# Optimization experiments

Measured on AMD Instinct MI355X. Metric: run time of the kernel, lower is better.

Reference implementation:

```python
import math
from itertools import product
import jax, jax.numpy as jnp
import numpy as np

# ---- static config (mirrors LPD.__init__) ----
IMG_W, IMG_H = 1920, 1080
MIN_SIZES = [[10, 16, 24], [32, 48], [64, 96], [128, 192, 256]]
STEPS = [8, 16, 32, 64]
VARIANCE = (0.1, 0.2)
CONF_THR = 0.3
NMS_THR = 0.3
TOP_K = 2000
KEEP_TOP_K = 750
BATCH = 16


def make_priors() -> np.ndarray:
    """Anchor grid in normalized (cx, cy, w, h), kornia _PriorBox order:
    per level, per cell (row-major), per min_size."""
    levels = []
    for step, mss in zip(STEPS, MIN_SIZES):
        fh, fw = math.ceil(IMG_H / step), math.ceil(IMG_W / step)
        ii, jj = np.meshgrid(np.arange(fh), np.arange(fw), indexing='ij')
        cx = (jj + 0.5) * step / IMG_W  # [fh, fw]
        cy = (ii + 0.5) * step / IMG_H
        nms_ = len(mss)
        cx = np.broadcast_to(cx[..., None], (fh, fw, nms_))
        cy = np.broadcast_to(cy[..., None], (fh, fw, nms_))
        skx = np.broadcast_to(np.array(mss, np.float64) / IMG_W, (fh, fw, nms_))
        sky = np.broadcast_to(np.array(mss, np.float64) / IMG_H, (fh, fw, nms_))
        levels.append(np.stack([cx, cy, skx, sky], -1).reshape(-1, 4))
    return np.concatenate(levels, 0).astype(np.float32)  # [N, 4]

N_PRIORS = make_priors().shape[0]  # 119130 for 1920x1080


def decode(loc, priors):
    """loc [B,N,14], priors [N,4] -> scaled [B,N,14] (x1y1x2y2 + 5 landmarks)."""
    var = jnp.asarray(VARIANCE, loc.dtype)
    p_xy, p_wh = priors[:, :2], priors[:, 2:4]
    cxcy = p_xy + loc[..., 0:2] * VARIANCE[0] * p_wh
    wh = p_wh * jnp.exp(loc[..., 2:4] * var)
    x1y1 = cxcy - wh * 0.5
    x2y2 = x1y1 + wh
    # 5 landmark points
    lmk = p_xy[None, :, None, :] + loc[..., 4:14].reshape(*loc.shape[:-1], 5, 2) * VARIANCE[0] * p_wh[None, :, None, :]
    boxes = jnp.concatenate([x1y1, x2y2, lmk.reshape(*loc.shape[:-1], 10)], -1)
    scale = jnp.tile(jnp.asarray([IMG_W, IMG_H], loc.dtype), 7)
    return boxes * scale


def nms_keep(b, s):
    """Greedy NMS. b [K,4] sorted by descending score s [K]. Returns bool keep [K]."""
    area = jnp.clip(b[:, 2] - b[:, 0], 0.0) * jnp.clip(b[:, 3] - b[:, 1], 0.0)
    lt = jnp.maximum(b[:, None, :2], b[None, :, :2])
    rb = jnp.minimum(b[:, None, 2:4], b[None, :, 2:4])
    whi = jnp.clip(rb - lt, 0.0)
    inter = whi[..., 0] * whi[..., 1]
    iou_m = inter / (area[:, None] + area[None, :] - inter + 1e-9)  # [K,K]
    K = b.shape[0]
    idx = jnp.arange(K)

    def step(active, i):
        keep_i = active[i]
        active = active & ~(keep_i & (iou_m[i] > NMS_THR) & (idx > i))
        return active, keep_i

    _, keep = jax.lax.scan(step, s > 0.0, idx)
    return keep


def setup_inputs() -> dict:
    key = jax.random.key(0)
    k1, k2, k3 = jax.random.split(key, 3)
    return {
        'loc': jax.random.normal(k1, (BATCH, N_PRIORS, 14), jnp.float32),
        'conf': jax.random.normal(k2, (BATCH, N_PRIORS, 2), jnp.float32),
        'iou': jax.random.normal(k3, (BATCH, N_PRIORS, 1), jnp.float32),
    }


def reference(loc, conf, iou):
    priors = jnp.asarray(make_priors())  # [N,4] constant
    cls = jax.nn.softmax(conf, axis=-1)[..., 1]          # [B,N]
    iou_s = jnp.clip(iou[..., 0], 0.0, 1.0)
    scores = jnp.sqrt(cls * iou_s)
    scores = jnp.where(scores >= CONF_THR, scores, 0.0)  # confidence threshold
    boxes = decode(loc, priors)                          # [B,N,14]
    top_s, top_i = jax.lax.top_k(scores, TOP_K)          # sorted desc
    boxes_k = jnp.take_along_axis(boxes, top_i[..., None], axis=1)  # [B,K,14]
    keep = jax.vmap(nms_keep)(boxes_k[..., :4], top_s)   # [B,K] bool
    keep = keep & (jnp.cumsum(keep.astype(jnp.int32), axis=-1) <= KEEP_TOP_K)
    dets = jnp.concatenate([boxes_k, (top_s * keep)[..., None]], -1)  # [B,K,15]
    return dets
```

## Files before the change

kernel.cpp:

```cpp
#include <hip/hip_runtime.h>
#include <math.h>

#define BB 16
#define TOPK 2000
#define KEEPK 750
#define CAND_CAP 4096
#define EDGE_CAP 8192
#define HIST_BINS 256
#define BIN_BASE 0x3E99u

__global__ __launch_bounds__(256) void k_scores(const float* __restrict__ conf,
                                                const float* __restrict__ iou,
                                                unsigned* __restrict__ sbits,
                                                unsigned* __restrict__ hist,
                                                unsigned* __restrict__ ccount,
                                                unsigned* __restrict__ ecount,
                                                int N, int nchunk) {
  __shared__ unsigned h[HIST_BINS];
  int b = blockIdx.y;
  int tid = threadIdx.x;
  for (int i = tid; i < HIST_BINS; i += 256) h[i] = 0;
  if (blockIdx.x == 0) {
    if (tid == 0) ccount[b] = 0;
    if (tid == 1) ecount[b] = 0;
  }
  __syncthreads();
  const float2* c2 = (const float2*)conf + (size_t)b * N;
  const float* iu = iou + (size_t)b * N;
  unsigned* sb = sbits + (size_t)b * N;
  int n0 = blockIdx.x * 4096;
#pragma unroll 4
  for (int k = 0; k < 16; ++k) {
    int n = n0 + k * 256 + tid;
    if (n < N) {
      float2 c = c2[n];
      float m = fmaxf(c.x, c.y);
      float e0 = (float)exp((double)(c.x - m));
      float e1 = (float)exp((double)(c.y - m));
      float p1 = e1 / (e0 + e1);
      float ic = fminf(fmaxf(iu[n], 0.0f), 1.0f);
      float s = sqrtf(p1 * ic);
      s = (s >= 0.3f) ? s : 0.0f;
      unsigned bits = __float_as_uint(s);
      sb[n] = bits;
      if (bits != 0u) {
        int bin = (int)(bits >> 16) - (int)BIN_BASE;
        bin = bin < 0 ? 0 : (bin > 255 ? 255 : bin);
        atomicAdd(&h[bin], 1u);
      }
    }
  }
  __syncthreads();
  unsigned* hdst = hist + ((size_t)b * nchunk + blockIdx.x) * HIST_BINS;
  for (int i = tid; i < HIST_BINS; i += 256) hdst[i] = h[i];
}

__global__ __launch_bounds__(256) void k_compact(const unsigned* __restrict__ sbits,
                                                 const unsigned* __restrict__ hist,
                                                 unsigned* __restrict__ ccount,
                                                 unsigned long long* __restrict__ ckeys,
                                                 int N, int nchunk) {
  __shared__ unsigned sT;
  __shared__ unsigned long long masks[32];
  __shared__ unsigned wioff[32];
  __shared__ unsigned blockbase;
  int b = blockIdx.y;
  int tid = threadIdx.x, lane = tid & 63, wv = tid >> 6;

  if (tid < 64) {
    const unsigned* h = hist + (size_t)b * nchunk * HIST_BINS;
    unsigned v0 = 0, v1 = 0, v2 = 0, v3 = 0;
    int b0 = 255 - (4 * lane + 0), b1 = 255 - (4 * lane + 1);
    int b2 = 255 - (4 * lane + 2), b3 = 255 - (4 * lane + 3);
    for (int c = 0; c < nchunk; ++c) {
      const unsigned* hc = h + c * HIST_BINS;
      v0 += hc[b0]; v1 += hc[b1]; v2 += hc[b2]; v3 += hc[b3];
    }
    unsigned p0 = v0, p1 = p0 + v1, p2 = p1 + v2, p3 = p2 + v3;
    unsigned tot = p3, pre = tot;
    for (int off = 1; off < 64; off <<= 1) {
      unsigned q = __shfl_up(pre, off);
      if (lane >= off) pre += q;
    }
    unsigned excl = pre - tot;
    int kk = -1;
    if (excl + p0 >= TOPK) kk = 0;
    else if (excl + p1 >= TOPK) kk = 1;
    else if (excl + p2 >= TOPK) kk = 2;
    else if (excl + p3 >= TOPK) kk = 3;
    unsigned long long m = __ballot(kk >= 0);
    int bin = 0;
    if (m != 0ull) {
      int fl = __ffsll((unsigned long long)m) - 1;
      int fk = __shfl(kk, fl);
      bin = 255 - (4 * fl + fk);
    }
    if (lane == 0) sT = ((unsigned)(BIN_BASE + (unsigned)bin)) << 16;
  }
  __syncthreads();
  unsigned T = sT;

  const unsigned* sb = sbits + (size_t)b * N;
  int n0 = blockIdx.x * 2048;
  unsigned v[8];
  unsigned long long mk[8];
#pragma unroll
  for (int k = 0; k < 8; ++k) {
    int n = n0 + k * 256 + tid;
    v[k] = (n < N) ? sb[n] : 0u;
    bool p = v[k] >= T;
    mk[k] = __ballot(p);
    if (lane == 0) masks[k * 4 + wv] = mk[k];
  }
  __syncthreads();
  if (tid < 64) {
    unsigned c = (tid < 32) ? (unsigned)__popcll(masks[tid]) : 0u;
    unsigned pre = c;
    for (int off = 1; off < 64; off <<= 1) {
      unsigned q = __shfl_up(pre, off);
      if (lane >= off) pre += q;
    }
    if (tid < 32) wioff[tid] = pre - c;
    if (tid == 31) blockbase = atomicAdd(&ccount[b], pre);
  }
  __syncthreads();
  unsigned base = blockbase;
#pragma unroll
  for (int k = 0; k < 8; ++k) {
    if ((mk[k] >> lane) & 1ull) {
      unsigned pos = base + wioff[k * 4 + wv] +
                     (unsigned)__popcll(mk[k] & ((1ull << lane) - 1ull));
      if (pos < CAND_CAP) {
        int n = n0 + k * 256 + tid;
        ckeys[(size_t)b * CAND_CAP + pos] =
            ((unsigned long long)v[k] << 32) | (unsigned)(~(unsigned)n);
      }
    }
  }
}

__global__ __launch_bounds__(256) void k_sort1(const unsigned* __restrict__ ccount,
                                               unsigned long long* __restrict__ ckeys) {
  __shared__ unsigned long long s[1024];
  int b = blockIdx.x >> 2, chunk = blockIdx.x & 3;
  bool asc = (chunk & 1) != 0;
  int t = threadIdx.x;
  unsigned c = ccount[b];
  if (c > CAND_CAP) c = CAND_CAP;
  unsigned long long* base = ckeys + (size_t)b * CAND_CAP + chunk * 1024;
  int goff = chunk * 1024;
  unsigned long long key[4];
#pragma unroll
  for (int e = 0; e < 4; ++e) {
    int g = goff + 4 * t + e;
    key[e] = (g < (int)c) ? base[4 * t + e] : 0ull;
  }
  for (int k = 2; k <= 1024; k <<= 1) {
    for (int j = k >> 1; j > 0; j >>= 1) {
      if (j >= 256) {
        __syncthreads();
#pragma unroll
        for (int e = 0; e < 4; ++e) s[4 * t + e] = key[e];
        __syncthreads();
        int pbase = (4 * t) ^ j;
        bool own_lo = ((4 * t) & j) == 0;
        bool dir = (((4 * t) & k) == 0) != asc;
        bool keep_max = (own_lo == dir);
#pragma unroll
        for (int e = 0; e < 4; ++e) {
          unsigned long long o = s[pbase + e];
          unsigned long long mx = key[e] > o ? key[e] : o;
          unsigned long long mn = key[e] > o ? o : key[e];
          key[e] = keep_max ? mx : mn;
        }
      } else if (j >= 4) {
        int d = j >> 2;
        bool own_lo = (t & d) == 0;
        bool dir = (((4 * t) & k) == 0) != asc;
        bool keep_max = (own_lo == dir);
#pragma unroll
        for (int e = 0; e < 4; ++e) {
          unsigned long long o = __shfl_xor(key[e], d, 64);
          unsigned long long mx = key[e] > o ? key[e] : o;
          unsigned long long mn = key[e] > o ? o : key[e];
          key[e] = keep_max ? mx : mn;
        }
      } else {
#pragma unroll
        for (int e = 0; e < 4; ++e) {
          int p = e ^ j;
          if (p > e) {
            int i = 4 * t + e;
            bool dir = (((i & k) == 0) != asc);
            bool need = dir ? (key[e] < key[p]) : (key[e] > key[p]);
            if (need) { unsigned long long tmp = key[e]; key[e] = key[p]; key[p] = tmp; }
          }
        }
      }
    }
  }
#pragma unroll
  for (int e = 0; e < 4; ++e) base[4 * t + e] = key[e];
}

__global__ __launch_bounds__(1024) void k_sort2_decode(
    const unsigned long long* __restrict__ ckeys, const float* __restrict__ loc,
    float* __restrict__ top_s, float* __restrict__ out,
    float4* __restrict__ boxes4, int N) {
  __shared__ unsigned long long s[CAND_CAP];
  int b = blockIdx.x;
  int t = threadIdx.x;
  const unsigned long long* src = ckeys + (size_t)b * CAND_CAP;
  unsigned long long key[4];
#pragma unroll
  for (int e = 0; e < 4; ++e) key[e] = src[4 * t + e];
  for (int k = 2048; k <= CAND_CAP; k <<= 1) {
    for (int j = k >> 1; j > 0; j >>= 1) {
      if (j >= 256) {
        __syncthreads();
#pragma unroll
        for (int e = 0; e < 4; ++e) s[4 * t + e] = key[e];
        __syncthreads();
        int pbase = (4 * t) ^ j;
        bool own_lo = ((4 * t) & j) == 0;
        bool dir = ((4 * t) & k) == 0;
        bool keep_max = (own_lo == dir);
#pragma unroll
        for (int e = 0; e < 4; ++e) {
          unsigned long long o = s[pbase + e];
          unsigned long long mx = key[e] > o ? key[e] : o;
          unsigned long long mn = key[e] > o ? o : key[e];
          key[e] = keep_max ? mx : mn;
        }
      } else if (j >= 4) {
        int d = j >> 2;
        bool own_lo = (t & d) == 0;
        bool dir = ((4 * t) & k) == 0;
        bool keep_max = (own_lo == dir);
#pragma unroll
        for (int e = 0; e < 4; ++e) {
          unsigned long long o = __shfl_xor(key[e], d, 64);
          unsigned long long mx = key[e] > o ? key[e] : o;
          unsigned long long mn = key[e] > o ? o : key[e];
          key[e] = keep_max ? mx : mn;
        }
      } else {
#pragma unroll
        for (int e = 0; e < 4; ++e) {
          int p = e ^ j;
          if (p > e) {
            int i = 4 * t + e;
            bool dir = ((i & k) == 0);
            bool need = dir ? (key[e] < key[p]) : (key[e] > key[p]);
            if (need) { unsigned long long tmp = key[e]; key[e] = key[p]; key[p] = tmp; }
          }
        }
      }
    }
  }
  if (t < TOPK / 4) {
#pragma unroll
    for (int e = 0; e < 4; ++e) {
      int r = 4 * t + e;
      unsigned long long kk = key[e];
      float sv = __uint_as_float((unsigned)(kk >> 32));
      top_s[b * TOPK + r] = sv;
      unsigned idxu = ~(unsigned)kk;
      if (idxu >= (unsigned)N) idxu = 0;
      int i = (int)idxu;
      int off, fw, st, nm, lvl;
      if (i < 97200)       { lvl = 0; off = 0;      fw = 240; st = 8;  nm = 3; }
      else if (i < 113520) { lvl = 1; off = 97200;  fw = 120; st = 16; nm = 2; }
      else if (i < 117600) { lvl = 2; off = 113520; fw = 60;  st = 32; nm = 2; }
      else                 { lvl = 3; off = 117600; fw = 30;  st = 64; nm = 3; }
      int tt = i - off;
      int cell = tt / nm;
      int kms = tt - cell * nm;
      int row = cell / fw;
      int col = cell - row * fw;
      int msv = (lvl == 0) ? (kms == 0 ? 10 : (kms == 1 ? 16 : 24))
              : (lvl == 1) ? (kms == 0 ? 32 : 48)
              : (lvl == 2) ? (kms == 0 ? 64 : 96)
                           : (kms == 0 ? 128 : (kms == 1 ? 192 : 256));
      float cx  = (float)(((double)col + 0.5) * (double)st / 1920.0);
      float cy  = (float)(((double)row + 0.5) * (double)st / 1080.0);
      float skx = (float)((double)msv / 1920.0);
      float sky = (float)((double)msv / 1080.0);
      const float2* lp2 = (const float2*)(loc + ((size_t)b * N + (size_t)i) * 14);
      float l[14];
#pragma unroll
      for (int q = 0; q < 7; ++q) { float2 v = lp2[q]; l[2 * q] = v.x; l[2 * q + 1] = v.y; }
      float cx2 = cx + (l[0] * 0.1f) * skx;
      float cy2 = cy + (l[1] * 0.1f) * sky;
      float wx = skx * expf(l[2] * 0.1f);
      float wy = sky * expf(l[3] * 0.2f);
      float x1 = cx2 - wx * 0.5f, y1 = cy2 - wy * 0.5f;
      float x2 = x1 + wx, y2 = y1 + wy;
      float X1 = x1 * 1920.0f, Y1 = y1 * 1080.0f, X2 = x2 * 1920.0f, Y2 = y2 * 1080.0f;
      float* o = out + ((size_t)b * TOPK + r) * 15;
      o[0] = X1; o[1] = Y1; o[2] = X2; o[3] = Y2;
#pragma unroll
      for (int q = 0; q < 5; ++q) {
        o[4 + 2 * q] = (cx + (l[4 + 2 * q] * 0.1f) * skx) * 1920.0f;
        o[5 + 2 * q] = (cy + (l[5 + 2 * q] * 0.1f) * sky) * 1080.0f;
      }
      boxes4[b * TOPK + r] = make_float4(X1, Y1, X2, Y2);
    }
  }
}

__global__ __launch_bounds__(128) void k_edges(const float4* __restrict__ boxes4,
                                               unsigned* __restrict__ ecount,
                                               unsigned* __restrict__ edges) {
  __shared__ float bx1[128], by1[128], bx2[128], by2[128], bta[128];
  __shared__ unsigned loc_e[1024];
  __shared__ unsigned lcnt, gbase;
  int b = blockIdx.y;
  int t = blockIdx.x;
  int it = 0;
  while ((it + 1) * (it + 2) / 2 <= t) ++it;
  int jt = t - it * (it + 1) / 2;
  int tid = threadIdx.x;
  if (tid == 0) lcnt = 0;
  int j0 = jt * 128;
  {
    int j = j0 + tid;
    if (j < TOPK) {
      float4 Bj = boxes4[b * TOPK + j];
      bx1[tid] = Bj.x; by1[tid] = Bj.y; bx2[tid] = Bj.z; by2[tid] = Bj.w;
      bta[tid] = 0.3f * (fmaxf(Bj.z - Bj.x, 0.f) * fmaxf(Bj.w - Bj.y, 0.f));
    } else {
      bx1[tid] = 1e30f; by1[tid] = 1e30f; bx2[tid] = -1e30f; by2[tid] = -1e30f;
      bta[tid] = 0.f;
    }
  }
  __syncthreads();
  int i = it * 128 + tid;
  int jmax = 0;
  float4 A4 = make_float4(0, 0, 0, 0);
  float taA = 0.f;
  if (i < TOPK) {
    A4 = boxes4[b * TOPK + i];
    taA = 0.3f * (fmaxf(A4.z - A4.x, 0.f) * fmaxf(A4.w - A4.y, 0.f));
    jmax = i - j0; if (jmax > 128) jmax = 128;
  }
  for (int c = 0; c < jmax; ++c) {
    float xx1 = fmaxf(A4.x, bx1[c]), yy1 = fmaxf(A4.y, by1[c]);
    float xx2 = fminf(A4.z, bx2[c]), yy2 = fminf(A4.w, by2[c]);
    float w = fmaxf(xx2 - xx1, 0.f), h = fmaxf(yy2 - yy1, 0.f);
    float inter = w * h;
    if (inter * 1.3f > taA + bta[c] + 3e-10f) {
      unsigned p = atomicAdd(&lcnt, 1u);
      if (p < 1024u) loc_e[p] = ((unsigned)i << 16) | (unsigned)(j0 + c);
    }
  }
  __syncthreads();
  unsigned cnt = lcnt > 1024u ? 1024u : lcnt;
  if (tid == 0 && cnt) gbase = atomicAdd(&ecount[b], cnt);
  __syncthreads();
  if (cnt) {
    unsigned* dst = edges + (size_t)b * EDGE_CAP;
    for (unsigned e = tid; e < cnt; e += 128) {
      unsigned p = gbase + e;
      if (p < EDGE_CAP) dst[p] = loc_e[e];
    }
  }
}

__global__ __launch_bounds__(256) void k_nms(const float* __restrict__ top_s,
                                             const unsigned* __restrict__ ecount,
                                             const unsigned* __restrict__ edges,
                                             float* __restrict__ out) {
  int b = blockIdx.x;
  __shared__ unsigned long long A[32], K[32], S[32];
  __shared__ unsigned pref[32];
  __shared__ unsigned ecache[4096];
  __shared__ int changed;
  int tid = threadIdx.x, lane = tid & 63, wv = tid >> 6;
  for (int base = 0; base < 2048; base += 256) {
    int i = base + tid;
    bool act = (i < TOPK) && (top_s[b * TOPK + i] > 0.0f);
    unsigned long long m = __ballot(act);
    if (lane == 0) { int w = (base >> 6) + wv; A[w] = m; K[w] = m; }
  }
  unsigned E = ecount[b];
  if (E > EDGE_CAP) E = EDGE_CAP;
  unsigned Ec = E > 4096u ? 4096u : E;
  for (unsigned e = tid; e < Ec; e += 256) ecache[e] = edges[(size_t)b * EDGE_CAP + e];
  __syncthreads();
  for (int it = 0; it < 32; ++it) {
    if (tid == 0) changed = 0;
    if (tid < 32) S[tid] = 0ull;
    __syncthreads();
    for (unsigned e = tid; e < Ec; e += 256) {
      unsigned v = ecache[e];
      unsigned i = v >> 16, j = v & 0xFFFFu;
      if ((K[j >> 6] >> (j & 63)) & 1ull) atomicOr(&S[i >> 6], 1ull << (i & 63));
    }
    for (unsigned e = 4096u + tid; e < E; e += 256) {
      unsigned v = edges[(size_t)b * EDGE_CAP + e];
      unsigned i = v >> 16, j = v & 0xFFFFu;
      if ((K[j >> 6] >> (j & 63)) & 1ull) atomicOr(&S[i >> 6], 1ull << (i & 63));
    }
    __syncthreads();
    if (tid < 32) {
      unsigned long long nk = A[tid] & ~S[tid];
      if (nk != K[tid]) { K[tid] = nk; changed = 1; }
    }
    __syncthreads();
    if (!changed) break;
  }
  if (tid == 0) {
    unsigned acc = 0;
    for (int w = 0; w < 32; ++w) { pref[w] = acc; acc += (unsigned)__popcll(K[w]); }
  }
  __syncthreads();
  for (int base = 0; base < 2048; base += 256) {
    int i = base + tid;
    if (i < TOPK) {
      int w = i >> 6;
      unsigned long long bit = (K[w] >> (i & 63)) & 1ull;
      unsigned rank = pref[w] + (unsigned)__popcll(K[w] & ((1ull << (i & 63)) - 1ull)) +
                      (unsigned)bit;
      float sv = top_s[b * TOPK + i];
      out[((size_t)b * TOPK + i) * 15 + 14] = (bit && rank <= KEEPK) ? sv : 0.0f;
    }
  }
}

extern "C" void kernel_launch(void* const* d_in, const int* in_sizes, int n_in,
                              void* d_out, int out_size, void* d_ws, size_t ws_size,
                              hipStream_t stream) {
  const float* loc  = (const float*)d_in[0];
  const float* conf = (const float*)d_in[1];
  const float* iou  = (const float*)d_in[2];
  float* out = (float*)d_out;
  int N = in_sizes[2] / BB;
  int nchunk = (N + 4095) / 4096;

  char* ws = (char*)d_ws;
  size_t off = 0;
  unsigned* ccount = (unsigned*)(ws + off); off += 64;
  unsigned* ecount = (unsigned*)(ws + off); off += 64;
  off = (off + 255) & ~(size_t)255;
  unsigned* hist   = (unsigned*)(ws + off); off += (size_t)BB * nchunk * HIST_BINS * 4;
  unsigned* sbits  = (unsigned*)(ws + off); off += (size_t)BB * N * 4;
  off = (off + 15) & ~(size_t)15;
  unsigned long long* ckeys = (unsigned long long*)(ws + off); off += (size_t)BB * CAND_CAP * 8;
  float* top_s = (float*)(ws + off);       off += (size_t)BB * TOPK * 4;
  off = (off + 15) & ~(size_t)15;
  float4* boxes4 = (float4*)(ws + off);    off += (size_t)BB * TOPK * 16;
  unsigned* edges = (unsigned*)(ws + off); off += (size_t)BB * EDGE_CAP * 4;

  k_scores<<<dim3(nchunk, BB), 256, 0, stream>>>(conf, iou, sbits, hist, ccount,
                                                 ecount, N, nchunk);
  k_compact<<<dim3((N + 2047) / 2048, BB), 256, 0, stream>>>(sbits, hist, ccount,
                                                             ckeys, N, nchunk);
  k_sort1<<<BB * 4, 256, 0, stream>>>(ccount, ckeys);
  k_sort2_decode<<<BB, 1024, 0, stream>>>(ckeys, loc, top_s, out, boxes4, N);
  k_edges<<<dim3(136, BB), 128, 0, stream>>>(boxes4, ecount, edges);
  k_nms<<<BB, 256, 0, stream>>>(top_s, ecount, edges, out);
}
```

Measured before the change: 270.2 us.

## Fuse edge construction and NMS via last-block atomic counter; spread decode across threads

```diff
diff --git a/kernel.cpp b/kernel.cpp
--- a/kernel.cpp
+++ b/kernel.cpp
@@ -15,6 +15,7 @@
                                                 unsigned* __restrict__ hist,
                                                 unsigned* __restrict__ ccount,
                                                 unsigned* __restrict__ ecount,
+                                                unsigned* __restrict__ tdone,
                                                 int N, int nchunk) {
   __shared__ unsigned h[HIST_BINS];
   int b = blockIdx.y;
@@ -23,6 +24,7 @@
   if (blockIdx.x == 0) {
     if (tid == 0) ccount[b] = 0;
     if (tid == 1) ecount[b] = 0;
+    if (tid == 2) tdone[b] = 0;
   }
   __syncthreads();
   const float2* c2 = (const float2*)conf + (size_t)b * N;
@@ -258,63 +260,67 @@
       }
     }
   }
-  if (t < TOPK / 4) {
-#pragma unroll
-    for (int e = 0; e < 4; ++e) {
-      int r = 4 * t + e;
-      unsigned long long kk = key[e];
-      float sv = __uint_as_float((unsigned)(kk >> 32));
-      top_s[b * TOPK + r] = sv;
-      unsigned idxu = ~(unsigned)kk;
-      if (idxu >= (unsigned)N) idxu = 0;
-      int i = (int)idxu;
-      int off, fw, st, nm, lvl;
-      if (i < 97200)       { lvl = 0; off = 0;      fw = 240; st = 8;  nm = 3; }
-      else if (i < 113520) { lvl = 1; off = 97200;  fw = 120; st = 16; nm = 2; }
-      else if (i < 117600) { lvl = 2; off = 113520; fw = 60;  st = 32; nm = 2; }
-      else                 { lvl = 3; off = 117600; fw = 30;  st = 64; nm = 3; }
-      int tt = i - off;
-      int cell = tt / nm;
-      int kms = tt - cell * nm;
-      int row = cell / fw;
-      int col = cell - row * fw;
-      int msv = (lvl == 0) ? (kms == 0 ? 10 : (kms == 1 ? 16 : 24))
-              : (lvl == 1) ? (kms == 0 ? 32 : 48)
-              : (lvl == 2) ? (kms == 0 ? 64 : 96)
-                           : (kms == 0 ? 128 : (kms == 1 ? 192 : 256));
-      float cx  = (float)(((double)col + 0.5) * (double)st / 1920.0);
-      float cy  = (float)(((double)row + 0.5) * (double)st / 1080.0);
-      float skx = (float)((double)msv / 1920.0);
-      float sky = (float)((double)msv / 1080.0);
-      const float2* lp2 = (const float2*)(loc + ((size_t)b * N + (size_t)i) * 14);
-      float l[14];
-#pragma unroll
-      for (int q = 0; q < 7; ++q) { float2 v = lp2[q]; l[2 * q] = v.x; l[2 * q + 1] = v.y; }
-      float cx2 = cx + (l[0] * 0.1f) * skx;
-      float cy2 = cy + (l[1] * 0.1f) * sky;
-      float wx = skx * expf(l[2] * 0.1f);
-      float wy = sky * expf(l[3] * 0.2f);
-      float x1 = cx2 - wx * 0.5f, y1 = cy2 - wy * 0.5f;
-      float x2 = x1 + wx, y2 = y1 + wy;
-      float X1 = x1 * 1920.0f, Y1 = y1 * 1080.0f, X2 = x2 * 1920.0f, Y2 = y2 * 1080.0f;
-      float* o = out + ((size_t)b * TOPK + r) * 15;
-      o[0] = X1; o[1] = Y1; o[2] = X2; o[3] = Y2;
-#pragma unroll
-      for (int q = 0; q < 5; ++q) {
-        o[4 + 2 * q] = (cx + (l[4 + 2 * q] * 0.1f) * skx) * 1920.0f;
-        o[5 + 2 * q] = (cy + (l[5 + 2 * q] * 0.1f) * sky) * 1080.0f;
-      }
-      boxes4[b * TOPK + r] = make_float4(X1, Y1, X2, Y2);
-    }
-  }
-}
-
-__global__ __launch_bounds__(128) void k_edges(const float4* __restrict__ boxes4,
-                                               unsigned* __restrict__ ecount,
-                                               unsigned* __restrict__ edges) {
+  __syncthreads();
+#pragma unroll
+  for (int e = 0; e < 4; ++e) s[4 * t + e] = key[e];
+  __syncthreads();
+  for (int r = t; r < TOPK; r += 1024) {
+    unsigned long long kk = s[r];
+    float sv = __uint_as_float((unsigned)(kk >> 32));
+    top_s[b * TOPK + r] = sv;
+    unsigned idxu = ~(unsigned)kk;
+    if (idxu >= (unsigned)N) idxu = 0;
+    int i = (int)idxu;
+    int off, fw, st, nm, lvl;
+    if (i < 97200)       { lvl = 0; off = 0;      fw = 240; st = 8;  nm = 3; }
+    else if (i < 113520) { lvl = 1; off = 97200;  fw = 120; st = 16; nm = 2; }
+    else if (i < 117600) { lvl = 2; off = 113520; fw = 60;  st = 32; nm = 2; }
+    else                 { lvl = 3; off = 117600; fw = 30;  st = 64; nm = 3; }
+    int tt = i - off;
+    int cell = tt / nm;
+    int kms = tt - cell * nm;
+    int row = cell / fw;
+    int col = cell - row * fw;
+    int msv = (lvl == 0) ? (kms == 0 ? 10 : (kms == 1 ? 16 : 24))
+            : (lvl == 1) ? (kms == 0 ? 32 : 48)
+            : (lvl == 2) ? (kms == 0 ? 64 : 96)
+                         : (kms == 0 ? 128 : (kms == 1 ? 192 : 256));
+    float cx  = (float)(((double)col + 0.5) * (double)st / 1920.0);
+    float cy  = (float)(((double)row + 0.5) * (double)st / 1080.0);
+    float skx = (float)((double)msv / 1920.0);
+    float sky = (float)((double)msv / 1080.0);
+    const float2* lp2 = (const float2*)(loc + ((size_t)b * N + (size_t)i) * 14);
+    float l[14];
+#pragma unroll
+    for (int q = 0; q < 7; ++q) { float2 v = lp2[q]; l[2 * q] = v.x; l[2 * q + 1] = v.y; }
+    float cx2 = cx + (l[0] * 0.1f) * skx;
+    float cy2 = cy + (l[1] * 0.1f) * sky;
+    float wx = skx * expf(l[2] * 0.1f);
+    float wy = sky * expf(l[3] * 0.2f);
+    float x1 = cx2 - wx * 0.5f, y1 = cy2 - wy * 0.5f;
+    float x2 = x1 + wx, y2 = y1 + wy;
+    float X1 = x1 * 1920.0f, Y1 = y1 * 1080.0f, X2 = x2 * 1920.0f, Y2 = y2 * 1080.0f;
+    float* o = out + ((size_t)b * TOPK + r) * 15;
+    o[0] = X1; o[1] = Y1; o[2] = X2; o[3] = Y2;
+#pragma unroll
+    for (int q = 0; q < 5; ++q) {
+      o[4 + 2 * q] = (cx + (l[4 + 2 * q] * 0.1f) * skx) * 1920.0f;
+      o[5 + 2 * q] = (cy + (l[5 + 2 * q] * 0.1f) * sky) * 1080.0f;
+    }
+    boxes4[b * TOPK + r] = make_float4(X1, Y1, X2, Y2);
+  }
+}
+
+__global__ __launch_bounds__(128) void k_edges_nms(const float4* __restrict__ boxes4,
+                                                   const float* __restrict__ top_s,
+                                                   unsigned* __restrict__ ecount,
+                                                   unsigned* __restrict__ edges,
+                                                   unsigned* __restrict__ tdone,
+                                                   float* __restrict__ out) {
   __shared__ float bx1[128], by1[128], bx2[128], by2[128], bta[128];
   __shared__ unsigned loc_e[1024];
   __shared__ unsigned lcnt, gbase;
+  __shared__ int is_last;
   int b = blockIdx.y;
   int t = blockIdx.x;
   int it = 0;
@@ -365,46 +371,49 @@
       if (p < EDGE_CAP) dst[p] = loc_e[e];
     }
   }
-}
-
-__global__ __launch_bounds__(256) void k_nms(const float* __restrict__ top_s,
-                                             const unsigned* __restrict__ ecount,
-                                             const unsigned* __restrict__ edges,
-                                             float* __restrict__ out) {
-  int b = blockIdx.x;
-  __shared__ unsigned long long A[32], K[32], S[32];
+  __syncthreads();
+  __threadfence();
+  if (tid == 0) {
+    unsigned done = atomicAdd(&tdone[b], 1u);
+    is_last = (done == 135u);
+  }
+  __syncthreads();
+  if (!is_last) return;
+  __threadfence();
+
+  __shared__ unsigned long long Am[32], K[32], S[32];
   __shared__ unsigned pref[32];
   __shared__ unsigned ecache[4096];
   __shared__ int changed;
-  int tid = threadIdx.x, lane = tid & 63, wv = tid >> 6;
-  for (int base = 0; base < 2048; base += 256) {
-    int i = base + tid;
-    bool act = (i < TOPK) && (top_s[b * TOPK + i] > 0.0f);
+  int lane = tid & 63, wv = tid >> 6;
+  for (int base = 0; base < 2048; base += 128) {
+    int i2 = base + tid;
+    bool act = (i2 < TOPK) && (top_s[b * TOPK + i2] > 0.0f);
     unsigned long long m = __ballot(act);
-    if (lane == 0) { int w = (base >> 6) + wv; A[w] = m; K[w] = m; }
+    if (lane == 0) { int w = (base >> 6) + wv; Am[w] = m; K[w] = m; }
   }
   unsigned E = ecount[b];
   if (E > EDGE_CAP) E = EDGE_CAP;
   unsigned Ec = E > 4096u ? 4096u : E;
-  for (unsigned e = tid; e < Ec; e += 256) ecache[e] = edges[(size_t)b * EDGE_CAP + e];
-  __syncthreads();
-  for (int it = 0; it < 32; ++it) {
+  for (unsigned e = tid; e < Ec; e += 128) ecache[e] = edges[(size_t)b * EDGE_CAP + e];
+  __syncthreads();
+  for (int iter = 0; iter < 32; ++iter) {
     if (tid == 0) changed = 0;
     if (tid < 32) S[tid] = 0ull;
     __syncthreads();
-    for (unsigned e = tid; e < Ec; e += 256) {
+    for (unsigned e = tid; e < Ec; e += 128) {
       unsigned v = ecache[e];
-      unsigned i = v >> 16, j = v & 0xFFFFu;
-      if ((K[j >> 6] >> (j & 63)) & 1ull) atomicOr(&S[i >> 6], 1ull << (i & 63));
-    }
-    for (unsigned e = 4096u + tid; e < E; e += 256) {
+      unsigned ii = v >> 16, j = v & 0xFFFFu;
+      if ((K[j >> 6] >> (j & 63)) & 1ull) atomicOr(&S[ii >> 6], 1ull << (ii & 63));
+    }
+    for (unsigned e = 4096u + tid; e < E; e += 128) {
       unsigned v = edges[(size_t)b * EDGE_CAP + e];
-      unsigned i = v >> 16, j = v & 0xFFFFu;
-      if ((K[j >> 6] >> (j & 63)) & 1ull) atomicOr(&S[i >> 6], 1ull << (i & 63));
+      unsigned ii = v >> 16, j = v & 0xFFFFu;
+      if ((K[j >> 6] >> (j & 63)) & 1ull) atomicOr(&S[ii >> 6], 1ull << (ii & 63));
     }
     __syncthreads();
     if (tid < 32) {
-      unsigned long long nk = A[tid] & ~S[tid];
+      unsigned long long nk = Am[tid] & ~S[tid];
       if (nk != K[tid]) { K[tid] = nk; changed = 1; }
     }
     __syncthreads();
@@ -415,15 +424,15 @@
     for (int w = 0; w < 32; ++w) { pref[w] = acc; acc += (unsigned)__popcll(K[w]); }
   }
   __syncthreads();
-  for (int base = 0; base < 2048; base += 256) {
-    int i = base + tid;
-    if (i < TOPK) {
-      int w = i >> 6;
-      unsigned long long bit = (K[w] >> (i & 63)) & 1ull;
-      unsigned rank = pref[w] + (unsigned)__popcll(K[w] & ((1ull << (i & 63)) - 1ull)) +
+  for (int base = 0; base < 2048; base += 128) {
+    int i2 = base + tid;
+    if (i2 < TOPK) {
+      int w = i2 >> 6;
+      unsigned long long bit = (K[w] >> (i2 & 63)) & 1ull;
+      unsigned rank = pref[w] + (unsigned)__popcll(K[w] & ((1ull << (i2 & 63)) - 1ull)) +
                       (unsigned)bit;
-      float sv = top_s[b * TOPK + i];
-      out[((size_t)b * TOPK + i) * 15 + 14] = (bit && rank <= KEEPK) ? sv : 0.0f;
+      float sv = top_s[b * TOPK + i2];
+      out[((size_t)b * TOPK + i2) * 15 + 14] = (bit && rank <= KEEPK) ? sv : 0.0f;
     }
   }
 }
@@ -442,6 +451,7 @@
   size_t off = 0;
   unsigned* ccount = (unsigned*)(ws + off); off += 64;
   unsigned* ecount = (unsigned*)(ws + off); off += 64;
+  unsigned* tdone  = (unsigned*)(ws + off); off += 64;
   off = (off + 255) & ~(size_t)255;
   unsigned* hist   = (unsigned*)(ws + off); off += (size_t)BB * nchunk * HIST_BINS * 4;
   unsigned* sbits  = (unsigned*)(ws + off); off += (size_t)BB * N * 4;
@@ -453,11 +463,10 @@
   unsigned* edges = (unsigned*)(ws + off); off += (size_t)BB * EDGE_CAP * 4;
 
   k_scores<<<dim3(nchunk, BB), 256, 0, stream>>>(conf, iou, sbits, hist, ccount,
-                                                 ecount, N, nchunk);
+                                                 ecount, tdone, N, nchunk);
   k_compact<<<dim3((N + 2047) / 2048, BB), 256, 0, stream>>>(sbits, hist, ccount,
                                                              ckeys, N, nchunk);
   k_sort1<<<BB * 4, 256, 0, stream>>>(ccount, ckeys);
   k_sort2_decode<<<BB, 1024, 0, stream>>>(ckeys, loc, top_s, out, boxes4, N);
-  k_edges<<<dim3(136, BB), 128, 0, stream>>>(boxes4, ecount, edges);
-  k_nms<<<BB, 256, 0, stream>>>(top_s, ecount, edges, out);
-}
+  k_edges_nms<<<dim3(136, BB), 128, 0, stream>>>(boxes4, top_s, ecount, edges, tdone, out);
+}
```

Result: slower. 336.7 us (+24.6%).
